# Performance work log

Measured on AMD Instinct MI355X. Metric: run time of the kernel, lower is better.

The kernel has to match this reference:

```python
import jax, jax.numpy as jnp
import numpy as np

N = 50000   # nodes
E = 800000  # edges
F_IN = 512
H = 128     # per-hop hidden width
ORDER = 3   # hops (iterations 1..3)
C = 16      # classes


def spmm(idx, vals, x):
    """Sparse [N,N] @ dense [N,d] via COO edges: out[r] += vals[e] * x[c]."""
    row, col = idx[0], idx[1]
    return jax.ops.segment_sum(vals[:, None] * x[col], row, num_segments=x.shape[0])


def setup_inputs() -> dict:
    key = jax.random.key(0)
    ks = jax.random.split(key, 9)
    x = jax.random.normal(ks[0], (N, F_IN), jnp.float32)
    adj_indices = jax.random.randint(ks[1], (2, E), 0, N)
    adj_values = jax.random.uniform(ks[2], (E,), jnp.float32)
    w1 = jax.random.normal(ks[3], (ORDER, F_IN, H), jnp.float32) * 0.05
    b1 = jax.random.normal(ks[4], (ORDER, 1, H), jnp.float32) * 0.05
    w2 = jax.random.normal(ks[5], (ORDER, ORDER * H, H), jnp.float32) * 0.05
    b2 = jax.random.normal(ks[6], (ORDER, 1, H), jnp.float32) * 0.05
    wf = jax.random.normal(ks[7], (ORDER * H, C), jnp.float32) * 0.05
    bf = jnp.zeros((C,), jnp.float32)
    return dict(x=x, adj_indices=adj_indices, adj_values=adj_values,
                w1=w1, b1=b1, w2=w2, b2=b2, wf=wf, bf=bf)


def reference(x, adj_indices, adj_values, w1, b1, w2, b2, wf, bf):
    # Upper: SparseNGCNLayer_i (iterations = i+1): XW + b -> relu -> (i) spmm hops.
    # Dropout is identity in eval mode.
    feats1 = []
    for i in range(ORDER):
        h = jax.nn.relu(x @ w1[i] + b1[i])  # [N, H]
        for _ in range(i):
            h = spmm(adj_indices, adj_values, h)
        feats1.append(h)
    a1 = jnp.concatenate(feats1, axis=1)  # [N, 3H]

    # Bottom: DenseNGCNLayer_i: AW -> (i) spmm hops -> + bias.
    feats2 = []
    for i in range(ORDER):
        h = a1 @ w2[i]  # [N, H]
        for _ in range(i):
            h = spmm(adj_indices, adj_values, h)
        feats2.append(h + b2[i])
    a2 = jnp.concatenate(feats2, axis=1)  # [N, 3H]

    return jax.nn.log_softmax(a2 @ wf + bf, axis=1)  # [N, C]
```

## Files before the change

kernel.cpp:

```cpp
#include <hip/hip_runtime.h>
#include <hip/hip_bf16.h>
#include <cstdint>
#include <cstddef>

#define N_NODES 50000
#define N_EDGES 800000
#define FIN 512
#define HW_ 128
#define NCLS 16
#define SCAN_NB 196

typedef __attribute__((ext_vector_type(4))) float floatx4;
typedef __attribute__((ext_vector_type(4))) int int4v;
typedef __bf16 bf16x8 __attribute__((ext_vector_type(8)));

__device__ __forceinline__ void glds16(const __bf16* g, __bf16* l) {
  __builtin_amdgcn_global_load_lds(
      (const __attribute__((address_space(1))) void*)g,
      (__attribute__((address_space(3))) void*)l, 16, 0, 0);
}

#define RP_NRANK 782
#define PREP_NT1 48
#define PREP_NU 120
__global__ __launch_bounds__(256) void k_rank_prep(
    const int* __restrict__ idx, int* __restrict__ cnt, int* __restrict__ rank,
    const float* __restrict__ w1, __bf16* __restrict__ w1t,
    const float* __restrict__ w2, const float* __restrict__ wf,
    __bf16* __restrict__ Ut,
    const float* __restrict__ b2, const float* __restrict__ bfv,
    float* __restrict__ cc) {
  int b = blockIdx.x;
  int tid = threadIdx.x;
  if (b < RP_NRANK) {
    int e = b * 1024 + tid;
#pragma unroll
    for (int u = 0; u < 4; u++) {
      int ee = e + u * 256;
      if (ee < N_EDGES) rank[ee] = atomicAdd(&cnt[idx[ee]], 1);
    }
  } else if (b < RP_NRANK + PREP_NT1) {
    int tb = b - RP_NRANK;
    const int K = FIN;
    int tilesK = K >> 6;
    int i = tb / (tilesK * 2);
    int rr = tb - i * tilesK * 2;
    int kt = rr >> 1;
    int nt = rr & 1;
    const float* wS = w1 + (size_t)i * K * 128;
    __bf16* wtS = w1t + (size_t)i * 128 * K;
    int k0 = kt * 64, n0 = nt * 64;
    __shared__ float tile[64][65];
    int tc = tid & 63, tr = tid >> 6;
#pragma unroll
    for (int q = 0; q < 16; q++) {
      int row = tr + q * 4;
      tile[row][tc] = wS[(size_t)(k0 + row) * 128 + n0 + tc];
    }
    __syncthreads();
#pragma unroll
    for (int q = 0; q < 16; q++) {
      int nr = tr + q * 4;
      wtS[(size_t)(n0 + nr) * K + k0 + tc] = (__bf16)tile[tc][nr];
    }
  } else if (b < RP_NRANK + PREP_NT1 + PREP_NU) {
    int t = (b - RP_NRANK - PREP_NT1) * 256 + tid;
    int col = t / 384;
    int q = t - col * 384;
    int p = col >> 4, c = col & 15;
    int j = q >> 7;
    int i = p - j;
    float val = 0.f;
    if (i >= 0 && i <= 2) {
      const float* w2row = w2 + ((size_t)i * 384 + q) * 128;
      const float* wfcol = wf + (size_t)128 * i * NCLS + c;
      for (int m = 0; m < 128; m++) val += w2row[m] * wfcol[m * NCLS];
    }
    Ut[(size_t)col * 384 + q] = (__bf16)val;
  } else {
    int c = tid;
    if (c < NCLS) {
      float s = bfv[c];
      for (int k = 0; k < 384; k++) s += b2[k] * wf[k * NCLS + c];
      cc[c] = s;
    }
  }
}

__global__ __launch_bounds__(256) void k_scan_block(const int* __restrict__ cnt,
                                                    int* __restrict__ bsum) {
  int t = blockIdx.x * 256 + threadIdx.x;
  int v = (t < N_NODES) ? cnt[t] : 0;
#pragma unroll
  for (int o = 32; o >= 1; o >>= 1) v += __shfl_down(v, o);
  __shared__ int ws[4];
  if ((threadIdx.x & 63) == 0) ws[threadIdx.x >> 6] = v;
  __syncthreads();
  if (threadIdx.x == 0) bsum[blockIdx.x] = ws[0] + ws[1] + ws[2] + ws[3];
}

__global__ __launch_bounds__(256) void k_scan_fill(const int* __restrict__ cnt,
                                                   const int* __restrict__ bsum,
                                                   int* __restrict__ rowptr) {
  int tid = threadIdx.x;
  int lane = tid & 63;
  int pv = (tid < blockIdx.x && tid < SCAN_NB) ? bsum[tid] : 0;
#pragma unroll
  for (int o = 32; o >= 1; o >>= 1) pv += __shfl_down(pv, o);
  __shared__ int ps[4];
  if (lane == 0) ps[tid >> 6] = pv;
  int t = blockIdx.x * 256 + tid;
  int c = (t < N_NODES) ? cnt[t] : 0;
  int v = c;
#pragma unroll
  for (int o = 1; o < 64; o <<= 1) {
    int n = __shfl_up(v, o);
    if (lane >= o) v += n;
  }
  __shared__ int wt[4];
  if (lane == 63) wt[tid >> 6] = v;
  __syncthreads();
  int add = ps[0] + ps[1] + ps[2] + ps[3];
  for (int w = 0; w < (tid >> 6); w++) add += wt[w];
  int ex = v - c + add;
  if (t < N_NODES) rowptr[t] = ex;
  if (t == 0) rowptr[N_NODES] = N_EDGES;
}

__global__ __launch_bounds__(256) void k_place(
    const int* __restrict__ idx, const float* __restrict__ vals,
    const int* __restrict__ rank, const int* __restrict__ rowptr,
    int2* __restrict__ epack) {
  int e = blockIdx.x * 256 + threadIdx.x;
  if (e < N_EDGES) {
    int r = idx[e];
    int c = idx[N_EDGES + e];
    int p = rowptr[r] + rank[e];
    epack[p] = make_int2(c, __float_as_int(vals[e]));
  }
}

#define G1_TRIOS 391
#define G1_TPX 49
__global__ __launch_bounds__(256) void gemm1(
    const float* __restrict__ A,
    const __bf16* __restrict__ Bt,
    const float* __restrict__ bias,
    __bf16* __restrict__ hb) {
  const int M = N_NODES, K = FIN;
  __shared__ __align__(16) __bf16 sA[2 * 128 * 32];
  __shared__ __align__(16) __bf16 sB[2 * 128 * 32];
  int tid = threadIdx.x;
  int id = blockIdx.x;
  int xcd = id & 7, slot = id >> 3;
  int trio = xcd * G1_TPX + slot / 3;
  int blk = slot - (slot / 3) * 3;
  if (trio >= G1_TRIOS) return;
  int m0 = trio * 128;
  const __bf16* Bblk = Bt + (size_t)blk * 128 * K;
  int wave = tid >> 6, lane = tid & 63;
  int wm = (wave & 1) * 64, wn = (wave >> 1) * 64;
  floatx4 acc[4][4] = {};

  int rA = lane >> 2;
  int gch = (lane & 3) ^ ((lane >> 3) & 3);
  int r0 = wave * 32 + rA;
  int r1 = r0 + 16;
  int gm0 = m0 + r0; gm0 = (gm0 < M) ? gm0 : (M - 1);
  int gm1 = m0 + r1; gm1 = (gm1 < M) ? gm1 : (M - 1);
  const float* pa0 = A + (size_t)gm0 * K + gch * 8;
  const float* pa1 = A + (size_t)gm1 * K + gch * 8;
  const __bf16* pb0 = Bblk + (size_t)r0 * K + gch * 8;
  const __bf16* pb1 = Bblk + (size_t)r1 * K + gch * 8;
  int lofsA = wave * 1024 + lane * 8;
  int lofsB = wave * 1024;

  int fm = lane & 15, fg = lane >> 4;
  int sloto = (fg ^ ((fm >> 1) & 3)) * 8;

  {
    floatx4 x0a = *(const floatx4*)(pa0);
    floatx4 x0b = *(const floatx4*)(pa0 + 4);
    floatx4 x1a = *(const floatx4*)(pa1);
    floatx4 x1b = *(const floatx4*)(pa1 + 4);
    glds16(pb0, sB + lofsB);
    glds16(pb1, sB + lofsB + 512);
    union { bf16x8 v; int4v i; } u0, u1;
#pragma unroll
    for (int q = 0; q < 4; q++) {
      u0.v[q] = (__bf16)x0a[q]; u0.v[q + 4] = (__bf16)x0b[q];
      u1.v[q] = (__bf16)x1a[q]; u1.v[q + 4] = (__bf16)x1b[q];
    }
    *(int4v*)(sA + lofsA) = u0.i;
    *(int4v*)(sA + lofsA + 512) = u1.i;
  }
  __syncthreads();

  for (int t = 0; t < 15; t++) {
    int cb = (t & 1) * 4096;
    int nb = cb ^ 4096;
    int k1 = t * 32 + 32;
    floatx4 n0a = *(const floatx4*)(pa0 + k1);
    floatx4 n0b = *(const floatx4*)(pa0 + k1 + 4);
    floatx4 n1a = *(const floatx4*)(pa1 + k1);
    floatx4 n1b = *(const floatx4*)(pa1 + k1 + 4);
    glds16(pb0 + k1, sB + nb + lofsB);
    glds16(pb1 + k1, sB + nb + lofsB + 512);

    bf16x8 af[4], bfr[4];
#pragma unroll
    for (int mt = 0; mt < 4; mt++)
      af[mt] = *(const bf16x8*)(sA + cb + (wm + mt * 16 + fm) * 32 + sloto);
#pragma unroll
    for (int nt = 0; nt < 4; nt++)
      bfr[nt] = *(const bf16x8*)(sB + cb + (wn + nt * 16 + fm) * 32 + sloto);
#pragma unroll
    for (int mt = 0; mt < 4; mt++)
#pragma unroll
      for (int nt = 0; nt < 4; nt++)
        acc[mt][nt] = __builtin_amdgcn_mfma_f32_16x16x32_bf16(af[mt], bfr[nt], acc[mt][nt], 0, 0, 0);

    union { bf16x8 v; int4v i; } u0, u1;
#pragma unroll
    for (int q = 0; q < 4; q++) {
      u0.v[q] = (__bf16)n0a[q]; u0.v[q + 4] = (__bf16)n0b[q];
      u1.v[q] = (__bf16)n1a[q]; u1.v[q + 4] = (__bf16)n1b[q];
    }
    *(int4v*)(sA + nb + lofsA) = u0.i;
    *(int4v*)(sA + nb + lofsA + 512) = u1.i;
    __syncthreads();
  }
  {
    int cb = 4096;
    bf16x8 af[4], bfr[4];
#pragma unroll
    for (int mt = 0; mt < 4; mt++)
      af[mt] = *(const bf16x8*)(sA + cb + (wm + mt * 16 + fm) * 32 + sloto);
#pragma unroll
    for (int nt = 0; nt < 4; nt++)
      bfr[nt] = *(const bf16x8*)(sB + cb + (wn + nt * 16 + fm) * 32 + sloto);
#pragma unroll
    for (int mt = 0; mt < 4; mt++)
#pragma unroll
      for (int nt = 0; nt < 4; nt++)
        acc[mt][nt] = __builtin_amdgcn_mfma_f32_16x16x32_bf16(af[mt], bfr[nt], acc[mt][nt], 0, 0, 0);
  }

  int colb = lane & 15, rbase = (lane >> 4) << 2;
#pragma unroll
  for (int mt = 0; mt < 4; mt++)
#pragma unroll
    for (int r = 0; r < 4; r++) {
      int gm = m0 + wm + mt * 16 + rbase + r;
      if (gm >= M) continue;
#pragma unroll
      for (int nt = 0; nt < 4; nt++) {
        int gc = blk * 128 + wn + nt * 16 + colb;
        float vv = acc[mt][nt][r] + bias[gc];
        vv = fmaxf(vv, 0.f);
        hb[(size_t)gm * 384 + gc] = (__bf16)vv;
      }
    }
}

__global__ __launch_bounds__(256) void k_sgemm(
    const __bf16* __restrict__ hb,
    const __bf16* __restrict__ Ut,
    float* __restrict__ S,
    float* __restrict__ R4) {
  const int M = N_NODES;
  int wave = threadIdx.x >> 6, lane = threadIdx.x & 63;
  int fm = lane & 15, fg = lane >> 4;
  int m0 = blockIdx.x * 128 + wave * 32;
  floatx4 acc[2][5] = {};
  int r0 = m0 + fm;      r0 = (r0 < M) ? r0 : (M - 1);
  int r1 = m0 + 16 + fm; r1 = (r1 < M) ? r1 : (M - 1);
  const __bf16* pa0 = hb + (size_t)r0 * 384 + fg * 8;
  const __bf16* pa1 = hb + (size_t)r1 * 384 + fg * 8;
  const __bf16* pb  = Ut + (size_t)fm * 384 + fg * 8;
#pragma unroll 2
  for (int k0 = 0; k0 < 384; k0 += 32) {
    bf16x8 a0 = *(const bf16x8*)(pa0 + k0);
    bf16x8 a1 = *(const bf16x8*)(pa1 + k0);
#pragma unroll
    for (int nt = 0; nt < 5; nt++) {
      bf16x8 bv = *(const bf16x8*)(pb + (size_t)nt * 16 * 384 + k0);
      acc[0][nt] = __builtin_amdgcn_mfma_f32_16x16x32_bf16(bv, a0, acc[0][nt], 0, 0, 0);
      acc[1][nt] = __builtin_amdgcn_mfma_f32_16x16x32_bf16(bv, a1, acc[1][nt], 0, 0, 0);
    }
  }
  int gm0 = m0 + fm;
  if (gm0 < M) {
#pragma unroll
    for (int nt = 0; nt < 4; nt++)
      *(floatx4*)(S + (size_t)nt * N_NODES * 16 + (size_t)gm0 * 16 + fg * 4) = acc[0][nt];
    *(floatx4*)(R4 + (size_t)gm0 * 16 + fg * 4) = acc[0][4];
  }
  int gm1 = m0 + 16 + fm;
  if (gm1 < M) {
#pragma unroll
    for (int nt = 0; nt < 4; nt++)
      *(floatx4*)(S + (size_t)nt * N_NODES * 16 + (size_t)gm1 * 16 + fg * 4) = acc[1][nt];
    *(floatx4*)(R4 + (size_t)gm1 * 16 + fg * 4) = acc[1][4];
  }
}

template <bool FINAL>
__global__ __launch_bounds__(256) void k_hop(
    const int* __restrict__ rowptr, const int2* __restrict__ epack,
    const float* __restrict__ Rin,
    const float* __restrict__ Sp,
    float* __restrict__ Rout,
    const float* __restrict__ cc) {
  int tid = threadIdx.x;
  int rg = tid >> 2, l = tid & 3;
  int row = blockIdx.x * 64 + rg;
  if (row >= N_NODES) return;
  int s = rowptr[row], e = rowptr[row + 1];
  floatx4 a = *(const floatx4*)(Sp + (size_t)row * 16 + l * 4);
  for (int i = s; i < e; i += 4) {
    int take = e - i; if (take > 4) take = 4;
    int2 ed = (l < take) ? epack[i + l] : make_int2(0, 0);
#pragma unroll
    for (int j = 0; j < 4; j++) {
      int c = __shfl(ed.x, j, 4);
      float v = __int_as_float(__shfl(ed.y, j, 4));
      floatx4 g = *(const floatx4*)(Rin + (size_t)c * 16 + l * 4);
      a += v * g;
    }
  }
  if (!FINAL) {
    *(floatx4*)(Rout + (size_t)row * 16 + l * 4) = a;
  } else {
    floatx4 ccv = *(const floatx4*)(cc + l * 4);
    a += ccv;
    float m = fmaxf(fmaxf(a[0], a[1]), fmaxf(a[2], a[3]));
    m = fmaxf(m, __shfl_xor(m, 1, 4));
    m = fmaxf(m, __shfl_xor(m, 2, 4));
    float sm = expf(a[0] - m) + expf(a[1] - m) + expf(a[2] - m) + expf(a[3] - m);
    sm += __shfl_xor(sm, 1, 4);
    sm += __shfl_xor(sm, 2, 4);
    float ls = logf(sm);
    floatx4 o;
#pragma unroll
    for (int q = 0; q < 4; q++) o[q] = (a[q] - m) - ls;
    *(floatx4*)(Rout + (size_t)row * 16 + l * 4) = o;
  }
}

extern "C" void kernel_launch(void* const* d_in, const int* in_sizes, int n_in,
                              void* d_out, int out_size, void* d_ws, size_t ws_size,
                              hipStream_t stream) {
  const float* x   = (const float*)d_in[0];
  const int*   adj = (const int*)d_in[1];
  const float* av  = (const float*)d_in[2];
  const float* w1  = (const float*)d_in[3];
  const float* b1  = (const float*)d_in[4];
  const float* w2  = (const float*)d_in[5];
  const float* b2  = (const float*)d_in[6];
  const float* wf  = (const float*)d_in[7];
  const float* bf  = (const float*)d_in[8];
  float* out = (float*)d_out;

  char* ws = (char*)d_ws;
  size_t off = 0;
  auto alloc = [&](size_t bytes) -> void* {
    off = (off + 255) & ~(size_t)255;
    void* p = ws + off;
    off += bytes;
    return p;
  };

  float* S    = (float*)alloc((size_t)N_NODES * 64 * 4);
  float* R4   = (float*)alloc((size_t)N_NODES * 16 * 4);
  float* RA   = (float*)alloc((size_t)N_NODES * 16 * 4);
  float* RB   = (float*)alloc((size_t)N_NODES * 16 * 4);
  __bf16* hb  = (__bf16*)alloc((size_t)N_NODES * 384 * 2);
  __bf16* w1t = (__bf16*)alloc((size_t)3 * 128 * FIN * 2);
  __bf16* Ut  = (__bf16*)alloc((size_t)80 * 384 * 2);
  int* rowptr = (int*)alloc((size_t)(N_NODES + 1) * 4);
  int* cnt    = (int*)alloc((size_t)N_NODES * 4);
  int* bsum   = (int*)alloc((size_t)SCAN_NB * 4);
  int* rankv  = (int*)alloc((size_t)N_EDGES * 4);
  int2* epack = (int2*)alloc((size_t)N_EDGES * 8);
  float* cc   = (float*)alloc(64);

  float* S0 = S;
  float* S1 = S + (size_t)N_NODES * 16;
  float* S2 = S + (size_t)N_NODES * 32;
  float* S3 = S + (size_t)N_NODES * 48;

  hipMemsetAsync(cnt, 0, (size_t)N_NODES * 4, stream);
  k_rank_prep<<<RP_NRANK + PREP_NT1 + PREP_NU + 1, 256, 0, stream>>>(
      adj, cnt, rankv, w1, w1t, w2, wf, Ut, b2, bf, cc);
  k_scan_block<<<SCAN_NB, 256, 0, stream>>>(cnt, bsum);
  k_scan_fill<<<SCAN_NB, 256, 0, stream>>>(cnt, bsum, rowptr);
  k_place<<<(N_EDGES + 255) / 256, 256, 0, stream>>>(adj, av, rankv, rowptr, epack);

  gemm1<<<8 * G1_TPX * 3, 256, 0, stream>>>(x, w1t, b1, hb);

  k_sgemm<<<(N_NODES + 127) / 128, 256, 0, stream>>>(hb, Ut, S, R4);

  int hop_grid = (N_NODES + 63) / 64;
  k_hop<false><<<hop_grid, 256, 0, stream>>>(rowptr, epack, R4, S3, RB, cc);
  k_hop<false><<<hop_grid, 256, 0, stream>>>(rowptr, epack, RB, S2, RA, cc);
  k_hop<false><<<hop_grid, 256, 0, stream>>>(rowptr, epack, RA, S1, RB, cc);
  k_hop<true><<<hop_grid, 256, 0, stream>>>(rowptr, epack, RB, S0, out, cc);
}
```

Measured before the change: 329.5 us.

## Drop per-edge rank array via atomic cursor placement; vectorize gemm1 epilogue stores

The count pass no longer stores a per-edge rank. Edge placement now claims slots with atomicAdd on a copy of rowptr, which removes the rank array's write and read traffic. Separately, gemm1 swaps the MFMA operand order so each lane holds four consecutive columns. The epilogue can then load the bias as a float4 and write four bf16 values in one 8-byte store instead of scattered 2-byte stores. The atomic placement makes the edge order within a row nondeterministic, so floating-point summation order in the hops can vary between runs.

```diff
diff --git a/kernel.cpp b/kernel.cpp
--- a/kernel.cpp
+++ b/kernel.cpp
@@ -12,6 +12,7 @@
 
 typedef __attribute__((ext_vector_type(4))) float floatx4;
 typedef __attribute__((ext_vector_type(4))) int int4v;
+typedef __attribute__((ext_vector_type(4))) short short4v;
 typedef __bf16 bf16x8 __attribute__((ext_vector_type(8)));
 
 __device__ __forceinline__ void glds16(const __bf16* g, __bf16* l) {
@@ -24,7 +25,7 @@
 #define PREP_NT1 48
 #define PREP_NU 120
 __global__ __launch_bounds__(256) void k_rank_prep(
-    const int* __restrict__ idx, int* __restrict__ cnt, int* __restrict__ rank,
+    const int* __restrict__ idx, int* __restrict__ cnt,
     const float* __restrict__ w1, __bf16* __restrict__ w1t,
     const float* __restrict__ w2, const float* __restrict__ wf,
     __bf16* __restrict__ Ut,
@@ -37,7 +38,7 @@
 #pragma unroll
     for (int u = 0; u < 4; u++) {
       int ee = e + u * 256;
-      if (ee < N_EDGES) rank[ee] = atomicAdd(&cnt[idx[ee]], 1);
+      if (ee < N_EDGES) atomicAdd(&cnt[idx[ee]], 1);
     }
   } else if (b < RP_NRANK + PREP_NT1) {
     int tb = b - RP_NRANK;
@@ -101,7 +102,8 @@
 
 __global__ __launch_bounds__(256) void k_scan_fill(const int* __restrict__ cnt,
                                                    const int* __restrict__ bsum,
-                                                   int* __restrict__ rowptr) {
+                                                   int* __restrict__ rowptr,
+                                                   int* __restrict__ rowptr_work) {
   int tid = threadIdx.x;
   int lane = tid & 63;
   int pv = (tid < blockIdx.x && tid < SCAN_NB) ? bsum[tid] : 0;
@@ -123,19 +125,19 @@
   int add = ps[0] + ps[1] + ps[2] + ps[3];
   for (int w = 0; w < (tid >> 6); w++) add += wt[w];
   int ex = v - c + add;
-  if (t < N_NODES) rowptr[t] = ex;
+  if (t < N_NODES) { rowptr[t] = ex; rowptr_work[t] = ex; }
   if (t == 0) rowptr[N_NODES] = N_EDGES;
 }
 
 __global__ __launch_bounds__(256) void k_place(
     const int* __restrict__ idx, const float* __restrict__ vals,
-    const int* __restrict__ rank, const int* __restrict__ rowptr,
+    int* __restrict__ rowptr_work,
     int2* __restrict__ epack) {
   int e = blockIdx.x * 256 + threadIdx.x;
   if (e < N_EDGES) {
     int r = idx[e];
     int c = idx[N_EDGES + e];
-    int p = rowptr[r] + rank[e];
+    int p = atomicAdd(&rowptr_work[r], 1);
     epack[p] = make_int2(c, __float_as_int(vals[e]));
   }
 }
@@ -218,7 +220,7 @@
     for (int mt = 0; mt < 4; mt++)
 #pragma unroll
       for (int nt = 0; nt < 4; nt++)
-        acc[mt][nt] = __builtin_amdgcn_mfma_f32_16x16x32_bf16(af[mt], bfr[nt], acc[mt][nt], 0, 0, 0);
+        acc[mt][nt] = __builtin_amdgcn_mfma_f32_16x16x32_bf16(bfr[nt], af[mt], acc[mt][nt], 0, 0, 0);
 
     union { bf16x8 v; int4v i; } u0, u1;
 #pragma unroll
@@ -243,24 +245,26 @@
     for (int mt = 0; mt < 4; mt++)
 #pragma unroll
       for (int nt = 0; nt < 4; nt++)
-        acc[mt][nt] = __builtin_amdgcn_mfma_f32_16x16x32_bf16(af[mt], bfr[nt], acc[mt][nt], 0, 0, 0);
-  }
-
-  int colb = lane & 15, rbase = (lane >> 4) << 2;
-#pragma unroll
-  for (int mt = 0; mt < 4; mt++)
-#pragma unroll
-    for (int r = 0; r < 4; r++) {
-      int gm = m0 + wm + mt * 16 + rbase + r;
+        acc[mt][nt] = __builtin_amdgcn_mfma_f32_16x16x32_bf16(bfr[nt], af[mt], acc[mt][nt], 0, 0, 0);
+  }
+
+#pragma unroll
+  for (int nt = 0; nt < 4; nt++) {
+    int gcb = blk * 128 + wn + nt * 16 + fg * 4;
+    floatx4 bv = *(const floatx4*)(bias + gcb);
+#pragma unroll
+    for (int mt = 0; mt < 4; mt++) {
+      int gm = m0 + wm + mt * 16 + fm;
       if (gm >= M) continue;
-#pragma unroll
-      for (int nt = 0; nt < 4; nt++) {
-        int gc = blk * 128 + wn + nt * 16 + colb;
-        float vv = acc[mt][nt][r] + bias[gc];
-        vv = fmaxf(vv, 0.f);
-        hb[(size_t)gm * 384 + gc] = (__bf16)vv;
+      union { short4v s; __bf16 h[4]; } o;
+#pragma unroll
+      for (int r = 0; r < 4; r++) {
+        float vv = acc[mt][nt][r] + bv[r];
+        o.h[r] = (__bf16)fmaxf(vv, 0.f);
       }
-    }
+      *(short4v*)(hb + (size_t)gm * 384 + gcb) = o.s;
+    }
+  }
 }
 
 __global__ __launch_bounds__(256) void k_sgemm(
@@ -379,9 +383,9 @@
   __bf16* w1t = (__bf16*)alloc((size_t)3 * 128 * FIN * 2);
   __bf16* Ut  = (__bf16*)alloc((size_t)80 * 384 * 2);
   int* rowptr = (int*)alloc((size_t)(N_NODES + 1) * 4);
+  int* rowptr_work = (int*)alloc((size_t)N_NODES * 4);
   int* cnt    = (int*)alloc((size_t)N_NODES * 4);
   int* bsum   = (int*)alloc((size_t)SCAN_NB * 4);
-  int* rankv  = (int*)alloc((size_t)N_EDGES * 4);
   int2* epack = (int2*)alloc((size_t)N_EDGES * 8);
   float* cc   = (float*)alloc(64);
 
@@ -392,10 +396,10 @@
 
   hipMemsetAsync(cnt, 0, (size_t)N_NODES * 4, stream);
   k_rank_prep<<<RP_NRANK + PREP_NT1 + PREP_NU + 1, 256, 0, stream>>>(
-      adj, cnt, rankv, w1, w1t, w2, wf, Ut, b2, bf, cc);
+      adj, cnt, w1, w1t, w2, wf, Ut, b2, bf, cc);
   k_scan_block<<<SCAN_NB, 256, 0, stream>>>(cnt, bsum);
-  k_scan_fill<<<SCAN_NB, 256, 0, stream>>>(cnt, bsum, rowptr);
-  k_place<<<(N_EDGES + 255) / 256, 256, 0, stream>>>(adj, av, rankv, rowptr, epack);
+  k_scan_fill<<<SCAN_NB, 256, 0, stream>>>(cnt, bsum, rowptr, rowptr_work);
+  k_place<<<(N_EDGES + 255) / 256, 256, 0, stream>>>(adj, av, rowptr_work, epack);
 
   gemm1<<<8 * G1_TPX * 3, 256, 0, stream>>>(x, w1t, b1, hb);
 
```

Measured after the change: 357.0 us. 8.3% more time.
